# Performance work log

Hardware: AMD Instinct MI355X
Metric: run time of the kernel (lower is better)

## Reference

```python
import jax, jax.numpy as jnp
import numpy as np

B, L, D, H = 2, 2048, 1024, 16
DH = D // H
EPS = 1e-5


def setup_inputs() -> dict:
    key = jax.random.key(0)
    ks = jax.random.split(key, 8)
    s = 0.02  # realistic init scale for weights
    # causal mask: True where attention is DISALLOWED (masked_fill semantics)
    mask = jnp.triu(jnp.ones((L, L), dtype=bool), k=1)[None, None]  # [1,1,L,L]
    return {
        "x": jax.random.normal(ks[0], (B, L, D), jnp.float32),
        "mask": mask,
        "ln_g": jnp.ones((D,), jnp.float32),
        "ln_b": jnp.zeros((D,), jnp.float32),
        "Wq": jax.random.normal(ks[1], (D, D), jnp.float32) * s,
        "bq": jnp.zeros((D,), jnp.float32),
        "Wk": jax.random.normal(ks[2], (D, D), jnp.float32) * s,
        "bk": jnp.zeros((D,), jnp.float32),
        "Wv": jax.random.normal(ks[3], (D, D), jnp.float32) * s,
        "bv": jnp.zeros((D,), jnp.float32),
        "Wo": jax.random.normal(ks[4], (D, D), jnp.float32) * s,
        "bo": jnp.zeros((D,), jnp.float32),
    }


def _layernorm(x, g, b):
    mu = jnp.mean(x, axis=-1, keepdims=True)
    var = jnp.var(x, axis=-1, keepdims=True)
    return (x - mu) * jax.lax.rsqrt(var + EPS) * g + b


def reference(x, mask, ln_g, ln_b, Wq, bq, Wk, bk, Wv, bv, Wo, bo):
    b, l, d = x.shape
    h = _layernorm(x, ln_g, ln_b)
    # separate Q/K/V linears, split into heads: [b, H, l, DH]
    q = (h @ Wq + bq).reshape(b, l, H, DH).transpose(0, 2, 1, 3)
    k = (h @ Wk + bk).reshape(b, l, H, DH).transpose(0, 2, 1, 3)
    v = (h @ Wv + bv).reshape(b, l, H, DH).transpose(0, 2, 1, 3)
    scale = jnp.asarray(DH, x.dtype) ** -0.5
    # full L x L score matrix (this is exactly what the torch module does)
    w = jnp.einsum("bhqd,bhkd->bhqk", q, k) * scale
    w = jnp.where(mask, -jnp.inf, w)
    w = jax.nn.softmax(w, axis=-1)
    # dropout layers are identity in eval mode
    o = jnp.einsum("bhqk,bhkd->bhqd", w, v)
    o = o.transpose(0, 2, 1, 3).reshape(b, l, d)
    return o @ Wo + bo
```

## Files before the change

kernel.cpp:

```cpp
#include <hip/hip_runtime.h>
#include <hip/hip_bf16.h>


typedef __bf16  bf16x8 __attribute__((ext_vector_type(8)));
typedef __bf16  bf16x4 __attribute__((ext_vector_type(4)));
typedef float   f32x4  __attribute__((ext_vector_type(4)));
typedef float   f32x16 __attribute__((ext_vector_type(16)));
typedef unsigned int u32x2 __attribute__((ext_vector_type(2)));
typedef unsigned int u32x4 __attribute__((ext_vector_type(4)));

#define MFMA16(a, b, c) __builtin_amdgcn_mfma_f32_16x16x32_bf16(a, b, c, 0, 0, 0)
#define MFMA32(a, b, c) __builtin_amdgcn_mfma_f32_32x32x16_bf16(a, b, c, 0, 0, 0)

#define LDT 72
#define LDO 68

#define QSCALE 0.18033688011112042f

__device__ __forceinline__ void gl_lds16(const void* g, void* l) {
    __builtin_amdgcn_global_load_lds(
        (const __attribute__((address_space(1))) void*)g,
        (__attribute__((address_space(3))) void*)l, 16, 0, 0);
}

__global__ __launch_bounds__(256) void ln_kernel(
    const float* __restrict__ x, const float* __restrict__ g,
    const float* __restrict__ bta, __hip_bfloat16* __restrict__ h)
{
    __shared__ float red[8];
    const int row = blockIdx.x, t = threadIdx.x;
    const float* xr = x + (size_t)row * 1024;
    const float4 xv = *(const float4*)(xr + t * 4);
    float s  = xv.x + xv.y + xv.z + xv.w;
    float ss = xv.x * xv.x + xv.y * xv.y + xv.z * xv.z + xv.w * xv.w;
    #pragma unroll
    for (int off = 32; off > 0; off >>= 1) {
        s  += __shfl_down(s, off);
        ss += __shfl_down(ss, off);
    }
    const int lane = t & 63, wave = t >> 6;
    if (lane == 0) { red[wave] = s; red[4 + wave] = ss; }
    __syncthreads();
    const float S  = red[0] + red[1] + red[2] + red[3];
    const float SS = red[4] + red[5] + red[6] + red[7];
    const float mu   = S * (1.0f / 1024.0f);
    const float var  = SS * (1.0f / 1024.0f) - mu * mu;
    const float rstd = rsqrtf(var + 1e-5f);
    const float4 gv = *(const float4*)(g + t * 4);
    const float4 bv = *(const float4*)(bta + t * 4);
    bf16x4 hv;
    hv[0] = (__bf16)((xv.x - mu) * rstd * gv.x + bv.x);
    hv[1] = (__bf16)((xv.y - mu) * rstd * gv.y + bv.y);
    hv[2] = (__bf16)((xv.z - mu) * rstd * gv.z + bv.z);
    hv[3] = (__bf16)((xv.w - mu) * rstd * gv.w + bv.w);
    *(bf16x4*)(h + (size_t)row * 1024 + t * 4) = hv;
}

__global__ void transpose_cast_kernel(
    const float* __restrict__ Wq, const float* __restrict__ Wk,
    const float* __restrict__ Wv, const float* __restrict__ Wo,
    __hip_bfloat16* __restrict__ tq, __hip_bfloat16* __restrict__ tk,
    __hip_bfloat16* __restrict__ tv, __hip_bfloat16* __restrict__ to_)
{
    __shared__ float t[32][33];
    const int z = blockIdx.z;
    const float* src = (z == 0) ? Wq : (z == 1) ? Wk : (z == 2) ? Wv : Wo;
    __hip_bfloat16* dst = (z == 0) ? tq : (z == 1) ? tk : (z == 2) ? tv : to_;
    const int n0 = blockIdx.x * 32, k0 = blockIdx.y * 32;
    const int tx = threadIdx.x, ty = threadIdx.y;
    t[ty][tx] = src[(size_t)(k0 + ty) * 1024 + n0 + tx];
    __syncthreads();
    dst[(size_t)(n0 + ty) * 1024 + k0 + tx] = __float2bfloat16(t[tx][ty]);
}

__device__ __forceinline__ void gemm_core_1024(
    const __hip_bfloat16* __restrict__ A, const __hip_bfloat16* __restrict__ Bt,
    int m0, int n0, f32x4 (&acc)[4][2])
{
    __shared__ __align__(16) __hip_bfloat16 sA[128 * 64];
    __shared__ __align__(16) __hip_bfloat16 sB[128 * 64];
    const int tid  = threadIdx.x;
    const int wave = tid >> 6, lane = tid & 63;
    const int quad = lane >> 4, l16 = lane & 15;
    const int wm = wave >> 2, wn = wave & 3;

    const f32x4 zero = {0.f, 0.f, 0.f, 0.f};
    #pragma unroll
    for (int i = 0; i < 4; ++i)
        #pragma unroll
        for (int j = 0; j < 2; ++j) acc[i][j] = zero;

    const int r0 = tid >> 3;
    const int c0 = (((tid & 7) ^ (r0 & 7)) << 3);
    const __hip_bfloat16* Ap = A  + (size_t)(m0 + r0) * 1024 + c0;
    const __hip_bfloat16* Bp = Bt + (size_t)(n0 + r0) * 1024 + c0;
    __hip_bfloat16* lA0 = sA + tid * 8;
    __hip_bfloat16* lB0 = sB + tid * 8;

    const int rsw = l16 & 7;

    for (int k0 = 0; k0 < 1024; k0 += 64) {
        __syncthreads();
        gl_lds16(Ap + k0, lA0);
        gl_lds16(Ap + (size_t)64 * 1024 + k0, lA0 + 64 * 64);
        gl_lds16(Bp + k0, lB0);
        gl_lds16(Bp + (size_t)64 * 1024 + k0, lB0 + 64 * 64);
        __syncthreads();
        #pragma unroll
        for (int kk = 0; kk < 64; kk += 32) {
            const int sl = (((quad + (kk >> 3)) ^ rsw) << 3);
            bf16x8 af[4], bfr[2];
            #pragma unroll
            for (int mt = 0; mt < 4; ++mt)
                af[mt] = *(const bf16x8*)(sA + (wm * 64 + mt * 16 + l16) * 64 + sl);
            #pragma unroll
            for (int nt = 0; nt < 2; ++nt)
                bfr[nt] = *(const bf16x8*)(sB + (wn * 32 + nt * 16 + l16) * 64 + sl);
            #pragma unroll
            for (int mt = 0; mt < 4; ++mt)
                #pragma unroll
                for (int nt = 0; nt < 2; ++nt)
                    acc[mt][nt] = MFMA16(af[mt], bfr[nt], acc[mt][nt]);
        }
    }
}

__global__ __launch_bounds__(512) void gemm_qkv_kernel(
    const __hip_bfloat16* __restrict__ h,
    const __hip_bfloat16* __restrict__ wt_base,
    const float* __restrict__ bq, const float* __restrict__ bk,
    const float* __restrict__ bv,
    __hip_bfloat16* __restrict__ qkv_base)
{
    const int z = blockIdx.z;
    const __hip_bfloat16* wt = wt_base + ((size_t)z << 20);
    __hip_bfloat16* outp = qkv_base + ((size_t)z << 22);

    const bool swp = (z == 2);
    const __hip_bfloat16* A  = swp ? wt : h;
    const __hip_bfloat16* Bt = swp ? h  : wt;
    const int m0 = swp ? blockIdx.x * 128 : blockIdx.y * 128;
    const int n0 = swp ? blockIdx.y * 128 : blockIdx.x * 128;

    f32x4 acc[4][2];
    gemm_core_1024(A, Bt, m0, n0, acc);

    const int lane = threadIdx.x & 63, wave = threadIdx.x >> 6;
    const int quad = lane >> 4, l16 = lane & 15;
    const int wm = wave >> 2, wn = wave & 3;

    if (!swp) {
        const float* bias = (z == 0) ? bq : bk;
        const float scale = (z == 0) ? QSCALE : 1.0f;
        #pragma unroll
        for (int mt = 0; mt < 4; ++mt)
            #pragma unroll
            for (int nt = 0; nt < 2; ++nt)
                #pragma unroll
                for (int r = 0; r < 4; ++r) {
                    const int gm = m0 + wm * 64 + mt * 16 + quad * 4 + r;
                    const int gn = n0 + wn * 32 + nt * 16 + l16;
                    const float v = (acc[mt][nt][r] + bias[gn]) * scale;
                    const int b = gm >> 11, l = gm & 2047;
                    const int hh = gn >> 6, dh = gn & 63;
                    outp[(((((size_t)(b * 16 + hh)) << 11) + l) * 64) + dh] = __float2bfloat16(v);
                }
    } else {
        #pragma unroll
        for (int mt = 0; mt < 4; ++mt)
            #pragma unroll
            for (int nt = 0; nt < 2; ++nt)
                #pragma unroll
                for (int r = 0; r < 4; ++r) {
                    const int rr = m0 + wm * 64 + mt * 16 + quad * 4 + r;
                    const int cc = n0 + wn * 32 + nt * 16 + l16;
                    const float v = acc[mt][nt][r] + bv[rr];
                    const int b = cc >> 11, l = cc & 2047;
                    const int hh = rr >> 6, dh = rr & 63;
                    outp[((((size_t)(b * 16 + hh)) * 64 + dh) << 11) + l] = __float2bfloat16(v);
                }
    }
}

__global__ __launch_bounds__(512) void gemm_out_kernel(
    const __hip_bfloat16* __restrict__ o, const __hip_bfloat16* __restrict__ wot,
    const float* __restrict__ bo, float* __restrict__ out)
{
    __shared__ __align__(16) __hip_bfloat16 sA[64 * 64];
    __shared__ __align__(16) __hip_bfloat16 sB[128 * 64];
    const int tid  = threadIdx.x;
    const int wave = tid >> 6, lane = tid & 63;
    const int quad = lane >> 4, l16 = lane & 15;
    const int wm = wave >> 2, wn = wave & 3;
    const int m0 = blockIdx.y * 64, n0 = blockIdx.x * 128;

    const f32x4 zero = {0.f, 0.f, 0.f, 0.f};
    f32x4 acc[2][2];
    #pragma unroll
    for (int i = 0; i < 2; ++i)
        #pragma unroll
        for (int j = 0; j < 2; ++j) acc[i][j] = zero;

    const int r0 = tid >> 3;
    const int c0 = (((tid & 7) ^ (r0 & 7)) << 3);
    const __hip_bfloat16* Ap = o   + (size_t)(m0 + r0) * 1024 + c0;
    const __hip_bfloat16* Bp = wot + (size_t)(n0 + r0) * 1024 + c0;
    __hip_bfloat16* lA0 = sA + tid * 8;
    __hip_bfloat16* lB0 = sB + tid * 8;

    const int rsw = l16 & 7;

    for (int k0 = 0; k0 < 1024; k0 += 64) {
        __syncthreads();
        gl_lds16(Ap + k0, lA0);
        gl_lds16(Bp + k0, lB0);
        gl_lds16(Bp + (size_t)64 * 1024 + k0, lB0 + 64 * 64);
        __syncthreads();
        #pragma unroll
        for (int kk = 0; kk < 64; kk += 32) {
            const int sl = (((quad + (kk >> 3)) ^ rsw) << 3);
            bf16x8 af[2], bfr[2];
            #pragma unroll
            for (int mt = 0; mt < 2; ++mt)
                af[mt] = *(const bf16x8*)(sA + (wm * 32 + mt * 16 + l16) * 64 + sl);
            #pragma unroll
            for (int nt = 0; nt < 2; ++nt)
                bfr[nt] = *(const bf16x8*)(sB + (wn * 32 + nt * 16 + l16) * 64 + sl);
            #pragma unroll
            for (int mt = 0; mt < 2; ++mt)
                #pragma unroll
                for (int nt = 0; nt < 2; ++nt)
                    acc[mt][nt] = MFMA16(af[mt], bfr[nt], acc[mt][nt]);
        }
    }

    #pragma unroll
    for (int mt = 0; mt < 2; ++mt)
        #pragma unroll
        for (int nt = 0; nt < 2; ++nt)
            #pragma unroll
            for (int r = 0; r < 4; ++r) {
                const int gm = m0 + wm * 32 + mt * 16 + quad * 4 + r;
                const int gn = n0 + wn * 32 + nt * 16 + l16;
                out[(size_t)gm * 1024 + gn] = acc[mt][nt][r] + bo[gn];
            }
}

__global__ __launch_bounds__(512, 4) void attn_kernel(
    const __hip_bfloat16* __restrict__ Q,
    const __hip_bfloat16* __restrict__ Kg,
    const __hip_bfloat16* __restrict__ Vt,
    __hip_bfloat16* __restrict__ O)
{
    __shared__ __align__(16) char smem[36864];
    __hip_bfloat16* sK = (__hip_bfloat16*)smem;
    __hip_bfloat16* sV = (__hip_bfloat16*)(smem + 18432);

    const int tid  = threadIdx.x;
    const int wave = tid >> 6, lane = tid & 63;
    const int grp  = wave >> 2, w4 = wave & 3;
    const int wk = w4 >> 1, wq = w4 & 1;
    const int q5 = lane & 31, hi = lane >> 5;
    const int bh = blockIdx.x, pi = blockIdx.y;
    const int qtA = 31 - pi, qtB = pi;
    const int q0A = qtA * 64, q0B = qtB * 64;

    const __hip_bfloat16* Qp = Q  + (size_t)bh * 2048 * 64;
    const __hip_bfloat16* Kp = Kg + (size_t)bh * 2048 * 64;
    const __hip_bfloat16* Vp = Vt + (size_t)bh * 64 * 2048;

    bf16x8 QfA[4], QfB[4];
    #pragma unroll
    for (int ks = 0; ks < 4; ++ks) {
        QfA[ks] = *(const bf16x8*)(Qp + (size_t)(q0A + wq * 32 + q5) * 64 + ks * 16 + hi * 8);
        QfB[ks] = *(const bf16x8*)(Qp + (size_t)(q0B + wq * 32 + q5) * 64 + ks * 16 + hi * 8);
    }

    f32x16 oA0, oA1, oB0, oB1;
    #pragma unroll
    for (int r = 0; r < 16; ++r) { oA0[r] = 0.f; oA1[r] = 0.f; oB0[r] = 0.f; oB1[r] = 0.f; }
    float lA = 0.f, lB = 0.f;

    const __hip_bfloat16* sKg = sK + grp * (64 * LDT);
    const __hip_bfloat16* sVg = sV + grp * (64 * LDT);
    const int qloc = wq * 32 + q5;

    const int sg = tid >> 8, tt = tid & 255;

    auto do_job = [&](const bf16x8 (&Qf)[4], float& l_run, bool diag,
                      f32x16& o0, f32x16& o1) {
        f32x16 s;
        #pragma unroll
        for (int i = 0; i < 16; ++i) s[i] = 0.f;
        __builtin_amdgcn_s_setprio(1);
        #pragma unroll
        for (int ks = 0; ks < 4; ++ks) {
            const bf16x8 kf = *(const bf16x8*)(sKg + (wk * 32 + q5) * LDT + ks * 16 + hi * 8);
            s = MFMA32(kf, Qf[ks], s);
        }
        __builtin_amdgcn_s_setprio(0);
        if (diag) {
            #pragma unroll
            for (int i = 0; i < 16; ++i) {
                const int krow = wk * 32 + (i & 3) + 8 * (i >> 2) + 4 * hi;
                if (krow > qloc) s[i] = -1e30f;
            }
        }
        float rs = 0.f;
        u32x2 U[4];
        #pragma unroll
        for (int rb = 0; rb < 4; ++rb) {
            bf16x4 pk;
            #pragma unroll
            for (int c = 0; c < 4; ++c) {
                const float p = exp2f(s[rb * 4 + c]);
                rs += p;
                pk[c] = (__bf16)p;
            }
            U[rb] = __builtin_bit_cast(u32x2, pk);
        }
        rs += __shfl_xor(rs, 32);
        l_run += rs;
        __builtin_amdgcn_s_setprio(1);
        #pragma unroll
        for (int t = 0; t < 2; ++t) {
            const unsigned p0a = __shfl_xor(U[2 * t][0], 32);
            const unsigned p0b = __shfl_xor(U[2 * t][1], 32);
            const unsigned p1a = __shfl_xor(U[2 * t + 1][0], 32);
            const unsigned p1b = __shfl_xor(U[2 * t + 1][1], 32);
            const unsigned w0 = hi ? p1a : U[2 * t][0];
            const unsigned w1 = hi ? p1b : U[2 * t][1];
            const unsigned w2 = hi ? U[2 * t + 1][0] : p0a;
            const unsigned w3 = hi ? U[2 * t + 1][1] : p0b;
            const u32x4 pw = {w0, w1, w2, w3};
            const bf16x8 pf = __builtin_bit_cast(bf16x8, pw);
            const bf16x8 vf0 = *(const bf16x8*)(sVg + (q5)      * LDT + wk * 32 + 16 * t + 8 * hi);
            const bf16x8 vf1 = *(const bf16x8*)(sVg + (32 + q5) * LDT + wk * 32 + 16 * t + 8 * hi);
            o0 = MFMA32(vf0, pf, o0);
            o1 = MFMA32(vf1, pf, o1);
        }
        __builtin_amdgcn_s_setprio(0);
    };

    for (int r = 0; r < 17; ++r) {
        __syncthreads();
        const int js = 2 * r + sg;
        if (js < 33) {
            const int ktS = (js <= qtA) ? js : js - qtA - 1;
            const int k0 = ktS * 64;
            __hip_bfloat16* dK = sK + sg * (64 * LDT);
            __hip_bfloat16* dV = sV + sg * (64 * LDT);
            #pragma unroll
            for (int i = 0; i < 2; ++i) {
                const int chunk = tt + 256 * i, rr = chunk >> 3, cc = (chunk & 7) << 3;
                *(int4*)(dK + rr * LDT + cc) = *(const int4*)(Kp + (size_t)(k0 + rr) * 64 + cc);
                *(int4*)(dV + rr * LDT + cc) = *(const int4*)(Vp + (size_t)rr * 2048 + k0 + cc);
            }
        }
        __syncthreads();

        const int j = 2 * r + grp;
        if (j < 33) {
            const bool isA = (j <= qtA);
            const int kt = isA ? j : j - qtA - 1;
            const bool diag = isA ? (kt == qtA) : (kt == qtB);
            if (isA) do_job(QfA, lA, diag, oA0, oA1);
            else     do_job(QfB, lB, diag, oB0, oB1);
        }
    }

    __syncthreads();
    float* Oscr = (float*)smem;
    float* lscr = (float*)(smem + 34816);

    if (hi == 0) {
        lscr[((0 * 2 + grp) * 2 + wk) * 64 + wq * 32 + q5] = lA;
        lscr[((1 * 2 + grp) * 2 + wk) * 64 + wq * 32 + q5] = lB;
    }

    auto wrO = [&](const f32x16& c0, const f32x16& c1, int t2, bool add) {
        float* rowp = Oscr + (t2 * 64 + wq * 32 + q5) * LDO;
        #pragma unroll
        for (int d = 0; d < 2; ++d) {
            const f32x16& oc = d ? c1 : c0;
            #pragma unroll
            for (int rb = 0; rb < 4; ++rb) {
                float* p = rowp + d * 32 + 8 * rb + 4 * hi;
                f32x4 v;
                if (add) {
                    v = *(const f32x4*)p;
                    v[0] += oc[rb * 4 + 0]; v[1] += oc[rb * 4 + 1];
                    v[2] += oc[rb * 4 + 2]; v[3] += oc[rb * 4 + 3];
                } else {
                    v[0] = oc[rb * 4 + 0]; v[1] = oc[rb * 4 + 1];
                    v[2] = oc[rb * 4 + 2]; v[3] = oc[rb * 4 + 3];
                }
                *(f32x4*)p = v;
            }
        }
    };
    if (grp == 1 && wk == 1) { wrO(oA0, oA1, 0, false); wrO(oB0, oB1, 1, false); }
    __syncthreads();
    if (grp == 1 && wk == 0) { wrO(oA0, oA1, 0, true);  wrO(oB0, oB1, 1, true); }
    __syncthreads();
    if (grp == 0 && wk == 1) { wrO(oA0, oA1, 0, true);  wrO(oB0, oB1, 1, true); }
    __syncthreads();
    if (grp == 0 && wk == 0) { wrO(oA0, oA1, 0, true);  wrO(oB0, oB1, 1, true); }
    __syncthreads();

    const int b = bh >> 4, hh = bh & 15;
    #pragma unroll
    for (int i = 0; i < 2; ++i) {
        const int chunk = tid + 512 * i;
        const int row = chunk >> 3, t2 = row >> 6, q = row & 63;
        const int col = (chunk & 7) << 3;
        const float lt = lscr[((t2 * 2 + 0) * 2 + 0) * 64 + q]
                       + lscr[((t2 * 2 + 0) * 2 + 1) * 64 + q]
                       + lscr[((t2 * 2 + 1) * 2 + 0) * 64 + q]
                       + lscr[((t2 * 2 + 1) * 2 + 1) * 64 + q];
        const float linv = 1.0f / lt;
        const float* src = Oscr + (t2 * 64 + q) * LDO + col;
        const f32x4 v0 = *(const f32x4*)src;
        const f32x4 v1 = *(const f32x4*)(src + 4);
        bf16x8 ov;
        ov[0] = (__bf16)(v0[0] * linv); ov[1] = (__bf16)(v0[1] * linv);
        ov[2] = (__bf16)(v0[2] * linv); ov[3] = (__bf16)(v0[3] * linv);
        ov[4] = (__bf16)(v1[0] * linv); ov[5] = (__bf16)(v1[1] * linv);
        ov[6] = (__bf16)(v1[2] * linv); ov[7] = (__bf16)(v1[3] * linv);
        const int q0X = t2 ? q0B : q0A;
        *(bf16x8*)(O + ((size_t)b * 2048 + q0X + q) * 1024 + hh * 64 + col) = ov;
    }
}

extern "C" void kernel_launch(void* const* d_in, const int* in_sizes, int n_in,
                              void* d_out, int out_size, void* d_ws, size_t ws_size,
                              hipStream_t stream) {
    const float* x    = (const float*)d_in[0];
    const float* ln_g = (const float*)d_in[2];
    const float* ln_b = (const float*)d_in[3];
    const float* Wq = (const float*)d_in[4];  const float* bq = (const float*)d_in[5];
    const float* Wk = (const float*)d_in[6];  const float* bk = (const float*)d_in[7];
    const float* Wv = (const float*)d_in[8];  const float* bv = (const float*)d_in[9];
    const float* Wo = (const float*)d_in[10]; const float* bo = (const float*)d_in[11];
    float* out = (float*)d_out;

    __hip_bfloat16* ws = (__hip_bfloat16*)d_ws;
    const size_t M1 = 1024 * 1024;
    __hip_bfloat16* h   = ws;
    __hip_bfloat16* wqt = ws + 4 * M1;
    __hip_bfloat16* wot = ws + 7 * M1;
    __hip_bfloat16* q   = ws + 8 * M1;
    __hip_bfloat16* k   = ws + 12 * M1;
    __hip_bfloat16* vt  = ws + 16 * M1;
    __hip_bfloat16* o   = h;

    ln_kernel<<<4096, 256, 0, stream>>>(x, ln_g, ln_b, h);
    transpose_cast_kernel<<<dim3(32, 32, 4), dim3(32, 32), 0, stream>>>(
        Wq, Wk, Wv, Wo, wqt, wqt + M1, wqt + 2 * M1, wot);
    gemm_qkv_kernel<<<dim3(8, 32, 3), 512, 0, stream>>>(h, wqt, bq, bk, bv, q);
    attn_kernel<<<dim3(32, 16), 512, 0, stream>>>(q, k, vt, o);
    gemm_out_kernel<<<dim3(8, 64), 512, 0, stream>>>(o, wot, bo, out);
}
```

Baseline: 222.8 us.

## Replace paired query-tile blocks with one query tile per block, longest-first

Previously each attention block handled two query tiles (31-pi and pi) so every block did a balanced 33 KV tiles. Now each block handles one 64-row query tile, the grid doubles to 32x32 blocks, and blockIdx.y maps to the largest tiles first so the scheduler can balance the uneven causal work. This raises parallelism and cuts register use, since there is only one Q fragment set and one pair of accumulators. In exchange, per-block work becomes uneven, there are twice as many K/V tile loads and epilogue reductions, and small blocks may leave one wave group idle in their last round.

```diff
diff --git a/kernel.cpp b/kernel.cpp
--- a/kernel.cpp
+++ b/kernel.cpp
@@ -261,95 +261,39 @@
     const int grp  = wave >> 2, w4 = wave & 3;
     const int wk = w4 >> 1, wq = w4 & 1;
     const int q5 = lane & 31, hi = lane >> 5;
-    const int bh = blockIdx.x, pi = blockIdx.y;
-    const int qtA = 31 - pi, qtB = pi;
-    const int q0A = qtA * 64, q0B = qtB * 64;
+    const int bh = blockIdx.x;
+    const int qt = 31 - blockIdx.y;
+    const int q0 = qt * 64;
 
     const __hip_bfloat16* Qp = Q  + (size_t)bh * 2048 * 64;
     const __hip_bfloat16* Kp = Kg + (size_t)bh * 2048 * 64;
     const __hip_bfloat16* Vp = Vt + (size_t)bh * 64 * 2048;
 
-    bf16x8 QfA[4], QfB[4];
-    #pragma unroll
-    for (int ks = 0; ks < 4; ++ks) {
-        QfA[ks] = *(const bf16x8*)(Qp + (size_t)(q0A + wq * 32 + q5) * 64 + ks * 16 + hi * 8);
-        QfB[ks] = *(const bf16x8*)(Qp + (size_t)(q0B + wq * 32 + q5) * 64 + ks * 16 + hi * 8);
-    }
-
-    f32x16 oA0, oA1, oB0, oB1;
-    #pragma unroll
-    for (int r = 0; r < 16; ++r) { oA0[r] = 0.f; oA1[r] = 0.f; oB0[r] = 0.f; oB1[r] = 0.f; }
-    float lA = 0.f, lB = 0.f;
+    bf16x8 Qf[4];
+    #pragma unroll
+    for (int ks = 0; ks < 4; ++ks)
+        Qf[ks] = *(const bf16x8*)(Qp + (size_t)(q0 + wq * 32 + q5) * 64 + ks * 16 + hi * 8);
+
+    f32x16 o0, o1;
+    #pragma unroll
+    for (int r = 0; r < 16; ++r) { o0[r] = 0.f; o1[r] = 0.f; }
+    float l_run = 0.f;
 
     const __hip_bfloat16* sKg = sK + grp * (64 * LDT);
     const __hip_bfloat16* sVg = sV + grp * (64 * LDT);
     const int qloc = wq * 32 + q5;
 
     const int sg = tid >> 8, tt = tid & 255;
-
-    auto do_job = [&](const bf16x8 (&Qf)[4], float& l_run, bool diag,
-                      f32x16& o0, f32x16& o1) {
-        f32x16 s;
-        #pragma unroll
-        for (int i = 0; i < 16; ++i) s[i] = 0.f;
-        __builtin_amdgcn_s_setprio(1);
-        #pragma unroll
-        for (int ks = 0; ks < 4; ++ks) {
-            const bf16x8 kf = *(const bf16x8*)(sKg + (wk * 32 + q5) * LDT + ks * 16 + hi * 8);
-            s = MFMA32(kf, Qf[ks], s);
-        }
-        __builtin_amdgcn_s_setprio(0);
-        if (diag) {
-            #pragma unroll
-            for (int i = 0; i < 16; ++i) {
-                const int krow = wk * 32 + (i & 3) + 8 * (i >> 2) + 4 * hi;
-                if (krow > qloc) s[i] = -1e30f;
-            }
-        }
-        float rs = 0.f;
-        u32x2 U[4];
-        #pragma unroll
-        for (int rb = 0; rb < 4; ++rb) {
-            bf16x4 pk;
-            #pragma unroll
-            for (int c = 0; c < 4; ++c) {
-                const float p = exp2f(s[rb * 4 + c]);
-                rs += p;
-                pk[c] = (__bf16)p;
-            }
-            U[rb] = __builtin_bit_cast(u32x2, pk);
-        }
-        rs += __shfl_xor(rs, 32);
-        l_run += rs;
-        __builtin_amdgcn_s_setprio(1);
-        #pragma unroll
-        for (int t = 0; t < 2; ++t) {
-            const unsigned p0a = __shfl_xor(U[2 * t][0], 32);
-            const unsigned p0b = __shfl_xor(U[2 * t][1], 32);
-            const unsigned p1a = __shfl_xor(U[2 * t + 1][0], 32);
-            const unsigned p1b = __shfl_xor(U[2 * t + 1][1], 32);
-            const unsigned w0 = hi ? p1a : U[2 * t][0];
-            const unsigned w1 = hi ? p1b : U[2 * t][1];
-            const unsigned w2 = hi ? U[2 * t + 1][0] : p0a;
-            const unsigned w3 = hi ? U[2 * t + 1][1] : p0b;
-            const u32x4 pw = {w0, w1, w2, w3};
-            const bf16x8 pf = __builtin_bit_cast(bf16x8, pw);
-            const bf16x8 vf0 = *(const bf16x8*)(sVg + (q5)      * LDT + wk * 32 + 16 * t + 8 * hi);
-            const bf16x8 vf1 = *(const bf16x8*)(sVg + (32 + q5) * LDT + wk * 32 + 16 * t + 8 * hi);
-            o0 = MFMA32(vf0, pf, o0);
-            o1 = MFMA32(vf1, pf, o1);
-        }
-        __builtin_amdgcn_s_setprio(0);
-    };
-
-    for (int r = 0; r < 17; ++r) {
+    __hip_bfloat16* dK = sK + sg * (64 * LDT);
+    __hip_bfloat16* dV = sV + sg * (64 * LDT);
+
+    const int R = (qt + 2) >> 1;
+
+    for (int r = 0; r < R; ++r) {
         __syncthreads();
         const int js = 2 * r + sg;
-        if (js < 33) {
-            const int ktS = (js <= qtA) ? js : js - qtA - 1;
-            const int k0 = ktS * 64;
-            __hip_bfloat16* dK = sK + sg * (64 * LDT);
-            __hip_bfloat16* dV = sV + sg * (64 * LDT);
+        if (js <= qt) {
+            const int k0 = js * 64;
             #pragma unroll
             for (int i = 0; i < 2; ++i) {
                 const int chunk = tt + 256 * i, rr = chunk >> 3, cc = (chunk & 7) << 3;
@@ -360,29 +304,74 @@
         __syncthreads();
 
         const int j = 2 * r + grp;
-        if (j < 33) {
-            const bool isA = (j <= qtA);
-            const int kt = isA ? j : j - qtA - 1;
-            const bool diag = isA ? (kt == qtA) : (kt == qtB);
-            if (isA) do_job(QfA, lA, diag, oA0, oA1);
-            else     do_job(QfB, lB, diag, oB0, oB1);
+        if (j <= qt) {
+            const bool diag = (j == qt);
+            f32x16 s;
+            #pragma unroll
+            for (int i = 0; i < 16; ++i) s[i] = 0.f;
+            __builtin_amdgcn_s_setprio(1);
+            #pragma unroll
+            for (int ks = 0; ks < 4; ++ks) {
+                const bf16x8 kf = *(const bf16x8*)(sKg + (wk * 32 + q5) * LDT + ks * 16 + hi * 8);
+                s = MFMA32(kf, Qf[ks], s);
+            }
+            __builtin_amdgcn_s_setprio(0);
+            if (diag) {
+                #pragma unroll
+                for (int i = 0; i < 16; ++i) {
+                    const int krow = wk * 32 + (i & 3) + 8 * (i >> 2) + 4 * hi;
+                    if (krow > qloc) s[i] = -1e30f;
+                }
+            }
+            float rs = 0.f;
+            u32x2 U[4];
+            #pragma unroll
+            for (int rb = 0; rb < 4; ++rb) {
+                bf16x4 pk;
+                #pragma unroll
+                for (int c = 0; c < 4; ++c) {
+                    const float p = exp2f(s[rb * 4 + c]);
+                    rs += p;
+                    pk[c] = (__bf16)p;
+                }
+                U[rb] = __builtin_bit_cast(u32x2, pk);
+            }
+            rs += __shfl_xor(rs, 32);
+            l_run += rs;
+            __builtin_amdgcn_s_setprio(1);
+            #pragma unroll
+            for (int t = 0; t < 2; ++t) {
+                const unsigned p0a = __shfl_xor(U[2 * t][0], 32);
+                const unsigned p0b = __shfl_xor(U[2 * t][1], 32);
+                const unsigned p1a = __shfl_xor(U[2 * t + 1][0], 32);
+                const unsigned p1b = __shfl_xor(U[2 * t + 1][1], 32);
+                const unsigned w0 = hi ? p1a : U[2 * t][0];
+                const unsigned w1 = hi ? p1b : U[2 * t][1];
+                const unsigned w2 = hi ? U[2 * t + 1][0] : p0a;
+                const unsigned w3 = hi ? U[2 * t + 1][1] : p0b;
+                const u32x4 pw = {w0, w1, w2, w3};
+                const bf16x8 pf = __builtin_bit_cast(bf16x8, pw);
+                const bf16x8 vf0 = *(const bf16x8*)(sVg + (q5)      * LDT + wk * 32 + 16 * t + 8 * hi);
+                const bf16x8 vf1 = *(const bf16x8*)(sVg + (32 + q5) * LDT + wk * 32 + 16 * t + 8 * hi);
+                o0 = MFMA32(vf0, pf, o0);
+                o1 = MFMA32(vf1, pf, o1);
+            }
+            __builtin_amdgcn_s_setprio(0);
         }
     }
 
     __syncthreads();
     float* Oscr = (float*)smem;
-    float* lscr = (float*)(smem + 34816);
-
-    if (hi == 0) {
-        lscr[((0 * 2 + grp) * 2 + wk) * 64 + wq * 32 + q5] = lA;
-        lscr[((1 * 2 + grp) * 2 + wk) * 64 + wq * 32 + q5] = lB;
-    }
-
-    auto wrO = [&](const f32x16& c0, const f32x16& c1, int t2, bool add) {
-        float* rowp = Oscr + (t2 * 64 + wq * 32 + q5) * LDO;
+    float* lscr = (float*)(smem + 17408);
+
+    if (hi == 0)
+        lscr[(grp * 2 + wk) * 64 + wq * 32 + q5] = l_run;
+
+    auto wrO = [&](bool add) {
+        float* rowp = Oscr + (wq * 32 + q5) * LDO;
         #pragma unroll
         for (int d = 0; d < 2; ++d) {
-            const f32x16& oc = d ? c1 : c0;
+            const f32x16& oc = d ? o1 : o0;
             #pragma unroll
             for (int rb = 0; rb < 4; ++rb) {
                 float* p = rowp + d * 32 + 8 * rb + 4 * hi;
@@ -399,37 +388,29 @@
             }
         }
     };
-    if (grp == 1 && wk == 1) { wrO(oA0, oA1, 0, false); wrO(oB0, oB1, 1, false); }
-    __syncthreads();
-    if (grp == 1 && wk == 0) { wrO(oA0, oA1, 0, true);  wrO(oB0, oB1, 1, true); }
-    __syncthreads();
-    if (grp == 0 && wk == 1) { wrO(oA0, oA1, 0, true);  wrO(oB0, oB1, 1, true); }
-    __syncthreads();
-    if (grp == 0 && wk == 0) { wrO(oA0, oA1, 0, true);  wrO(oB0, oB1, 1, true); }
+    if (grp == 1 && wk == 1) wrO(false);
+    __syncthreads();
+    if (grp == 1 && wk == 0) wrO(true);
+    __syncthreads();
+    if (grp == 0 && wk == 1) wrO(true);
+    __syncthreads();
+    if (grp == 0 && wk == 0) wrO(true);
     __syncthreads();
 
     const int b = bh >> 4, hh = bh & 15;
-    #pragma unroll
-    for (int i = 0; i < 2; ++i) {
-        const int chunk = tid + 512 * i;
-        const int row = chunk >> 3, t2 = row >> 6, q = row & 63;
-        const int col = (chunk & 7) << 3;
-        const float lt = lscr[((t2 * 2 + 0) * 2 + 0) * 64 + q]
-                       + lscr[((t2 * 2 + 0) * 2 + 1) * 64 + q]
-                       + lscr[((t2 * 2 + 1) * 2 + 0) * 64 + q]
-                       + lscr[((t2 * 2 + 1) * 2 + 1) * 64 + q];
-        const float linv = 1.0f / lt;
-        const float* src = Oscr + (t2 * 64 + q) * LDO + col;
-        const f32x4 v0 = *(const f32x4*)src;
-        const f32x4 v1 = *(const f32x4*)(src + 4);
-        bf16x8 ov;
-        ov[0] = (__bf16)(v0[0] * linv); ov[1] = (__bf16)(v0[1] * linv);
-        ov[2] = (__bf16)(v0[2] * linv); ov[3] = (__bf16)(v0[3] * linv);
-        ov[4] = (__bf16)(v1[0] * linv); ov[5] = (__bf16)(v1[1] * linv);
-        ov[6] = (__bf16)(v1[2] * linv); ov[7] = (__bf16)(v1[3] * linv);
-        const int q0X = t2 ? q0B : q0A;
-        *(bf16x8*)(O + ((size_t)b * 2048 + q0X + q) * 1024 + hh * 64 + col) = ov;
-    }
+    const int row = tid >> 3, col = (tid & 7) << 3;
+    const float lt = lscr[(0 * 2 + 0) * 64 + row] + lscr[(0 * 2 + 1) * 64 + row]
+                   + lscr[(1 * 2 + 0) * 64 + row] + lscr[(1 * 2 + 1) * 64 + row];
+    const float linv = 1.0f / lt;
+    const float* src = Oscr + row * LDO + col;
+    const f32x4 v0 = *(const f32x4*)src;
+    const f32x4 v1 = *(const f32x4*)(src + 4);
+    bf16x8 ov;
+    ov[0] = (__bf16)(v0[0] * linv); ov[1] = (__bf16)(v0[1] * linv);
+    ov[2] = (__bf16)(v0[2] * linv); ov[3] = (__bf16)(v0[3] * linv);
+    ov[4] = (__bf16)(v1[0] * linv); ov[5] = (__bf16)(v1[1] * linv);
+    ov[6] = (__bf16)(v1[2] * linv); ov[7] = (__bf16)(v1[3] * linv);
+    *(bf16x8*)(O + ((size_t)b * 2048 + q0 + row) * 1024 + hh * 64 + col) = ov;
 }
 
 extern "C" void kernel_launch(void* const* d_in, const int* in_sizes, int n_in,
@@ -458,6 +439,6 @@
     transpose_cast_kernel<<<dim3(32, 32, 4), dim3(32, 32), 0, stream>>>(
         Wq, Wk, Wv, Wo, wqt, wqt + M1, wqt + 2 * M1, wot);
     gemm_qkv_kernel<<<dim3(8, 32, 3), 512, 0, stream>>>(h, wqt, bq, bk, bv, q);
-    attn_kernel<<<dim3(32, 16), 512, 0, stream>>>(q, k, vt, o);
+    attn_kernel<<<dim3(32, 32), 512, 0, stream>>>(q, k, vt, o);
     gemm_out_kernel<<<dim3(8, 64), 512, 0, stream>>>(o, wot, bo, out);
 }
```

Result: faster. 198.5 us (-10.9%).
